# Kernel tuning notes

Hardware: AMD Instinct MI355X
Metric: run time of the kernel (lower is better)

Reference implementation:

```python
import jax, jax.numpy as jnp
import numpy as np

B, S_SRC, L_SRC, S_TGT, L_TGT, C = 4, 8, 512, 8, 512, 4
K_PALETTE = 97
PAD = -1.0
TAU = 0.1
EPS = 1e-15


def setup_inputs() -> dict:
    key = jax.random.key(0)
    k1, k2, k3, k4, k5, k6 = jax.random.split(key, 6)
    palette = jax.random.uniform(k1, (K_PALETTE, C), dtype=jnp.float32)
    src_idx = jax.random.randint(k2, (B, S_SRC, L_SRC), 0, K_PALETTE)
    tgt_idx = jax.random.randint(k3, (B, S_TGT, L_TGT), 0, K_PALETTE)
    src = palette[src_idx]
    tgt = palette[tgt_idx]
    pad_vec = jnp.full((C,), PAD, dtype=jnp.float32)
    src = jnp.where(jax.random.uniform(k4, (B, S_SRC, L_SRC, 1)) < 0.03, pad_vec, src)
    tgt = jnp.where(jax.random.uniform(k5, (B, S_TGT, L_TGT, 1)) < 0.03, pad_vec, tgt)
    seg_sim_map = jax.random.normal(k6, (B, S_TGT * L_TGT, S_SRC * L_SRC), dtype=jnp.float32)
    return {"seg_sim_map": seg_sim_map, "seg_colors_src": src, "seg_colors_tgt": tgt}


def _loss(seg_sim_map, seg_colors_src, seg_colors_tgt):
    Bb = seg_sim_map.shape[0]
    src_flat = seg_colors_src.reshape(Bb, -1, C)   # [B, Nsrc, C]
    tgt_flat = seg_colors_tgt.reshape(Bb, -1, C)   # [B, Ntgt, C]
    valid_src = ~jnp.all(src_flat == PAD, axis=-1)  # [B, Nsrc]
    valid_tgt = ~jnp.all(tgt_flat == PAD, axis=-1)  # [B, Ntgt]

    # eq[b,t,j]: valid tgt row t's color exactly equals valid src column j's color.
    # This replaces torch.unique + index_add: aggregating softmax mass over src
    # positions sharing the gt color is identical to index_add by color index
    # followed by gathering the gt color's bucket.
    eq = jnp.all(tgt_flat[:, :, None, :] == src_flat[:, None, :, :], axis=-1)
    eq = eq & valid_src[:, None, :] & valid_tgt[:, :, None]      # [B, Ntgt, Nsrc]
    matched = jnp.any(eq, axis=-1)                               # rows kept by nll mask

    # masked softmax over valid src columns == softmax over the sliced columns
    logits = jnp.where(valid_src[:, None, :], seg_sim_map / TAU, -jnp.inf)
    probs = jax.nn.softmax(logits, axis=-1)                      # [B, Ntgt, Nsrc]

    p_gt = jnp.einsum('btj,btj->bt', probs, eq.astype(probs.dtype))
    nll = -jnp.log(p_gt + EPS)                                   # [B, Ntgt]

    nll = nll.reshape(Bb, S_TGT, L_TGT)
    m = matched.reshape(Bb, S_TGT, L_TGT).astype(nll.dtype)
    nvalid = m.sum(-1)                                           # [B, S_tgt]
    seg_loss = jnp.where(nvalid > 0, (nll * m).sum(-1) / jnp.maximum(nvalid, 1.0), 0.0)
    cnt = jnp.sum((nvalid > 0).astype(jnp.int32))
    total = seg_loss.sum() / jnp.maximum(cnt, 1).astype(seg_loss.dtype)
    return total, cnt


def reference(seg_sim_map, seg_colors_src, seg_colors_tgt):
    return _loss(seg_sim_map, seg_colors_src, seg_colors_tgt)
```

## Files before the change

### kernel.cpp

```cpp
#include <hip/hip_runtime.h>
#include <math.h>

#define NSRC 4096
#define NTGT 4096
#define NB 4
#define L2SCALE (10.0f * 1.4426950408889634f)
#define PADBITS 0xBF800000u


__device__ __forceinline__ unsigned mix128(uint4 c) {
    unsigned h = c.x * 0x9E3779B1u;
    h ^= h >> 15; h *= 0x85EBCA77u;
    h ^= c.y;     h *= 0xC2B2AE3Du;
    h ^= h >> 13;
    h ^= c.z;     h *= 0x27D4EB2Fu;
    h ^= h >> 16;
    h ^= c.w;     h *= 0x9E3779B1u;
    h ^= h >> 15;
    return h;
}

__global__ __launch_bounds__(256) void key_kernel(const uint4* __restrict__ srcc,
                                                  const uint4* __restrict__ tgtc,
                                                  unsigned* __restrict__ skey,
                                                  unsigned* __restrict__ tkey) {
    int i = blockIdx.x * 256 + threadIdx.x;
    if (i < NB * NSRC) {
        uint4 c = srcc[i];
        bool pad = (c.x == PADBITS) && (c.y == PADBITS) && (c.z == PADBITS) && (c.w == PADBITS);
        skey[i] = pad ? 0u : (mix128(c) | 1u);
    } else {
        int j = i - NB * NSRC;
        uint4 c = tgtc[j];
        bool pad = (c.x == PADBITS) && (c.y == PADBITS) && (c.z == PADBITS) && (c.w == PADBITS);
        tkey[j] = pad ? 2u : (mix128(c) | 1u);
    }
}


__global__ __launch_bounds__(256) void row_kernel(const float* __restrict__ sim,
                                                  const unsigned* __restrict__ skey,
                                                  const unsigned* __restrict__ tkey,
                                                  float* __restrict__ row_nll,
                                                  float* __restrict__ row_m) {
    const int wave = threadIdx.x >> 6;
    const int lane = threadIdx.x & 63;
    const int row = blockIdx.x * 4 + wave;
    const int b = row >> 12;
    const float4* simv = (const float4*)(sim + (size_t)row * NSRC);
    const uint4* keyv = (const uint4*)(skey + (size_t)b * NSRC);
    const unsigned tk = tkey[row];

    float s0 = 0.f, s1 = 0.f, s2 = 0.f, s3 = 0.f;
    float g0 = 0.f, g1 = 0.f, g2 = 0.f, g3 = 0.f;
    int any = 0;

#define PROC(LV, KV, SA, GA)                                             \
    do {                                                                 \
        bool _eq = ((KV) == tk);                                         \
        float _arg = ((KV) != 0u) ? (LV) * L2SCALE : -1048576.0f;        \
        float _e = exp2f(_arg);                                          \
        SA += _e;                                                        \
        GA += _eq ? _e : 0.f;                                            \
        any |= (int)_eq;                                                 \
    } while (0)

    #pragma unroll
    for (int it = 0; it < 16; ++it) {
        int j4 = it * 64 + lane;
        float4 l4 = simv[j4];
        uint4 k4 = keyv[j4];
        PROC(l4.x, k4.x, s0, g0);
        PROC(l4.y, k4.y, s1, g1);
        PROC(l4.z, k4.z, s2, g2);
        PROC(l4.w, k4.w, s3, g3);
    }
#undef PROC

    float s = (s0 + s1) + (s2 + s3);
    float sg = (g0 + g1) + (g2 + g3);
    #pragma unroll
    for (int off = 1; off < 64; off <<= 1) {
        s += __shfl_xor(s, off);
        sg += __shfl_xor(sg, off);
    }
    any = __any(any) ? 1 : 0;

    if (lane == 0) {
        float p = (s > 0.f) ? (sg / s) : 0.f;
        float nll = -logf(p + 1e-15f);
        row_nll[row] = any ? nll : 0.f;
        row_m[row] = any ? 1.f : 0.f;
    }
}


__global__ __launch_bounds__(1024) void finalize_kernel(const float* __restrict__ row_nll,
                                                        const float* __restrict__ row_m,
                                                        float* __restrict__ out) {
    __shared__ float ssum[32], scnt[32];
    int wave = threadIdx.x >> 6, lane = threadIdx.x & 63;
    for (int seg = wave; seg < 32; seg += 16) {
        float a = 0.f, c = 0.f;
        for (int j = lane; j < 512; j += 64) {
            a += row_nll[seg * 512 + j];
            c += row_m[seg * 512 + j];
        }
        #pragma unroll
        for (int off = 1; off < 64; off <<= 1) {
            a += __shfl_xor(a, off);
            c += __shfl_xor(c, off);
        }
        if (lane == 0) { ssum[seg] = a; scnt[seg] = c; }
    }
    __syncthreads();
    if (threadIdx.x == 0) {
        float tot = 0.f;
        int cnt = 0;
        for (int i = 0; i < 32; ++i) {
            if (scnt[i] > 0.f) { tot += ssum[i] / scnt[i]; cnt++; }
        }
        out[0] = (cnt > 0) ? tot / (float)cnt : 0.f;
        out[1] = (float)cnt;
    }
}


extern "C" void kernel_launch(void* const* d_in, const int* in_sizes, int n_in,
                              void* d_out, int out_size, void* d_ws, size_t ws_size,
                              hipStream_t stream) {
    const float* sim = (const float*)d_in[0];
    const uint4* src = (const uint4*)d_in[1];
    const uint4* tgt = (const uint4*)d_in[2];
    float* out = (float*)d_out;

    unsigned* skey = (unsigned*)d_ws;
    unsigned* tkey = skey + NB * NSRC;
    float* row_nll = (float*)(tkey + NB * NTGT);
    float* row_m = row_nll + NB * NTGT;

    key_kernel<<<(NB * (NSRC + NTGT)) / 256, 256, 0, stream>>>(src, tgt, skey, tkey);
    row_kernel<<<NB * NTGT / 4, 256, 0, stream>>>(sim, skey, tkey, row_nll, row_m);
    finalize_kernel<<<1, 1024, 0, stream>>>(row_nll, row_m, out);
}
```

Before: 59.77 us.

## Stream sim with nontemporal loads and accumulate per-segment sums via atomics

The row kernel now reads the similarity matrix with nontemporal loads in a partially unrolled loop, since that data is read only once. Instead of writing per-row nll and mask arrays, each matched row atomically adds into 32 per-segment accumulators, which the key kernel zeroes. This shrinks the finalize kernel to a single wave. It reduces intermediate traffic and finalize work, but adds float atomic contention and makes the summation order nondeterministic.

```diff
diff --git a/kernel.cpp b/kernel.cpp
--- a/kernel.cpp
+++ b/kernel.cpp
@@ -6,6 +6,8 @@
 #define NB 4
 #define L2SCALE (10.0f * 1.4426950408889634f)
 #define PADBITS 0xBF800000u
+
+typedef float f4v __attribute__((ext_vector_type(4)));
 
 
 __device__ __forceinline__ unsigned mix128(uint4 c) {
@@ -23,8 +25,10 @@
 __global__ __launch_bounds__(256) void key_kernel(const uint4* __restrict__ srcc,
                                                   const uint4* __restrict__ tgtc,
                                                   unsigned* __restrict__ skey,
-                                                  unsigned* __restrict__ tkey) {
+                                                  unsigned* __restrict__ tkey,
+                                                  float* __restrict__ seg_acc) {
     int i = blockIdx.x * 256 + threadIdx.x;
+    if (blockIdx.x == 0 && threadIdx.x < 64) seg_acc[threadIdx.x] = 0.f;
     if (i < NB * NSRC) {
         uint4 c = srcc[i];
         bool pad = (c.x == PADBITS) && (c.y == PADBITS) && (c.z == PADBITS) && (c.w == PADBITS);
@@ -41,13 +45,12 @@
 __global__ __launch_bounds__(256) void row_kernel(const float* __restrict__ sim,
                                                   const unsigned* __restrict__ skey,
                                                   const unsigned* __restrict__ tkey,
-                                                  float* __restrict__ row_nll,
-                                                  float* __restrict__ row_m) {
+                                                  float* __restrict__ seg_acc) {
     const int wave = threadIdx.x >> 6;
     const int lane = threadIdx.x & 63;
     const int row = blockIdx.x * 4 + wave;
     const int b = row >> 12;
-    const float4* simv = (const float4*)(sim + (size_t)row * NSRC);
+    const f4v* simv = (const f4v*)(sim + (size_t)row * NSRC);
     const uint4* keyv = (const uint4*)(skey + (size_t)b * NSRC);
     const unsigned tk = tkey[row];
 
@@ -65,15 +68,18 @@
         any |= (int)_eq;                                                 \
     } while (0)
 
-    #pragma unroll
-    for (int it = 0; it < 16; ++it) {
-        int j4 = it * 64 + lane;
-        float4 l4 = simv[j4];
-        uint4 k4 = keyv[j4];
-        PROC(l4.x, k4.x, s0, g0);
-        PROC(l4.y, k4.y, s1, g1);
-        PROC(l4.z, k4.z, s2, g2);
-        PROC(l4.w, k4.w, s3, g3);
+    #pragma unroll 1
+    for (int it = 0; it < 4; ++it) {
+        #pragma unroll
+        for (int u = 0; u < 4; ++u) {
+            int j4 = it * 256 + u * 64 + lane;
+            f4v l4 = __builtin_nontemporal_load(&simv[j4]);
+            uint4 k4 = keyv[j4];
+            PROC(l4[0], k4.x, s0, g0);
+            PROC(l4[1], k4.y, s1, g1);
+            PROC(l4[2], k4.z, s2, g2);
+            PROC(l4[3], k4.w, s3, g3);
+        }
     }
 #undef PROC
 
@@ -86,42 +92,33 @@
     }
     any = __any(any) ? 1 : 0;
 
-    if (lane == 0) {
+    if (lane == 0 && any) {
         float p = (s > 0.f) ? (sg / s) : 0.f;
         float nll = -logf(p + 1e-15f);
-        row_nll[row] = any ? nll : 0.f;
-        row_m[row] = any ? 1.f : 0.f;
+        int seg = row >> 9;
+        atomicAdd(&seg_acc[seg], nll);
+        atomicAdd(&seg_acc[32 + seg], 1.f);
     }
 }
 
 
-__global__ __launch_bounds__(1024) void finalize_kernel(const float* __restrict__ row_nll,
-                                                        const float* __restrict__ row_m,
-                                                        float* __restrict__ out) {
-    __shared__ float ssum[32], scnt[32];
-    int wave = threadIdx.x >> 6, lane = threadIdx.x & 63;
-    for (int seg = wave; seg < 32; seg += 16) {
-        float a = 0.f, c = 0.f;
-        for (int j = lane; j < 512; j += 64) {
-            a += row_nll[seg * 512 + j];
-            c += row_m[seg * 512 + j];
-        }
-        #pragma unroll
-        for (int off = 1; off < 64; off <<= 1) {
-            a += __shfl_xor(a, off);
-            c += __shfl_xor(c, off);
-        }
-        if (lane == 0) { ssum[seg] = a; scnt[seg] = c; }
+__global__ __launch_bounds__(64) void finalize_kernel(const float* __restrict__ seg_acc,
+                                                      float* __restrict__ out) {
+    int lane = threadIdx.x;
+    float loss = 0.f, flag = 0.f;
+    if (lane < 32) {
+        float sum = seg_acc[lane];
+        float cnt = seg_acc[32 + lane];
+        if (cnt > 0.f) { loss = sum / cnt; flag = 1.f; }
     }
-    __syncthreads();
-    if (threadIdx.x == 0) {
-        float tot = 0.f;
-        int cnt = 0;
-        for (int i = 0; i < 32; ++i) {
-            if (scnt[i] > 0.f) { tot += ssum[i] / scnt[i]; cnt++; }
-        }
-        out[0] = (cnt > 0) ? tot / (float)cnt : 0.f;
-        out[1] = (float)cnt;
+    #pragma unroll
+    for (int off = 1; off < 64; off <<= 1) {
+        loss += __shfl_xor(loss, off);
+        flag += __shfl_xor(flag, off);
+    }
+    if (lane == 0) {
+        out[0] = (flag > 0.f) ? loss / flag : 0.f;
+        out[1] = flag;
     }
 }
 
@@ -136,10 +133,9 @@
 
     unsigned* skey = (unsigned*)d_ws;
     unsigned* tkey = skey + NB * NSRC;
-    float* row_nll = (float*)(tkey + NB * NTGT);
-    float* row_m = row_nll + NB * NTGT;
+    float* seg_acc = (float*)(tkey + NB * NTGT);
 
-    key_kernel<<<(NB * (NSRC + NTGT)) / 256, 256, 0, stream>>>(src, tgt, skey, tkey);
-    row_kernel<<<NB * NTGT / 4, 256, 0, stream>>>(sim, skey, tkey, row_nll, row_m);
-    finalize_kernel<<<1, 1024, 0, stream>>>(row_nll, row_m, out);
+    key_kernel<<<(NB * (NSRC + NTGT)) / 256, 256, 0, stream>>>(src, tgt, skey, tkey, seg_acc);
+    row_kernel<<<NB * NTGT / 4, 256, 0, stream>>>(sim, skey, tkey, seg_acc);
+    finalize_kernel<<<1, 64, 0, stream>>>(seg_acc, out);
 }
```

Measured after the change: 220.4 us. +268.8%, slower.

## Bucket source columns by color hash and gather matching columns per row

Applied to the files above, without the earlier changes.

Replaces the per-element key comparison with a per-batch shared-memory hash table that groups source column indices by color, built by one block per batch. Each row now computes the unmasked exp sum over all columns without loading keys. It then gathers only the columns of its matching color bucket and of the pad bucket to get the gt mass and to subtract the pad mass. Padded target rows exit early. This removes the key-array loads and the per-element selects, and uses the raw hardware exp2 builtin. The trade-offs are a serial single-block build stage, scattered gathers, and a 256-slot table that assumes few distinct colors per batch.

```diff
diff --git a/kernel.cpp b/kernel.cpp
--- a/kernel.cpp
+++ b/kernel.cpp
@@ -7,6 +7,7 @@
 #define L2SCALE (10.0f * 1.4426950408889634f)
 #define PADBITS 0xBF800000u
 
+__device__ __forceinline__ float fexp2(float x) { return __builtin_amdgcn_exp2f(x); }
 
 __device__ __forceinline__ unsigned mix128(uint4 c) {
     unsigned h = c.x * 0x9E3779B1u;
@@ -17,78 +18,136 @@
     h ^= h >> 16;
     h ^= c.w;     h *= 0x9E3779B1u;
     h ^= h >> 15;
-    return h;
-}
-
-__global__ __launch_bounds__(256) void key_kernel(const uint4* __restrict__ srcc,
+    return h | 1u;
+}
+
+
+__global__ __launch_bounds__(1024) void build_kernel(const uint4* __restrict__ srcc,
+                                                     unsigned* __restrict__ cols,
+                                                     unsigned* __restrict__ gkey,
+                                                     unsigned* __restrict__ gstart,
+                                                     unsigned* __restrict__ gcnt) {
+    const int b = blockIdx.x;
+    const int tid = threadIdx.x;
+    __shared__ unsigned hkey[256];
+    __shared__ int hcnt[256], hstart[256], hfill[256];
+    __shared__ int padcnt, padfill;
+    if (tid < 256) { hkey[tid] = 0u; hcnt[tid] = 0; hfill[tid] = 0; }
+    if (tid == 0) { padcnt = 0; padfill = 0; }
+    __syncthreads();
+
+    int slotreg[4];
+    #pragma unroll
+    for (int u = 0; u < 4; ++u) {
+        int j = u * 1024 + tid;
+        uint4 c = srcc[b * NSRC + j];
+        bool pad = (c.x == PADBITS) && (c.y == PADBITS) && (c.z == PADBITS) && (c.w == PADBITS);
+        if (pad) {
+            slotreg[u] = -1;
+            atomicAdd(&padcnt, 1);
+        } else {
+            unsigned k = mix128(c);
+            int s = (k >> 8) & 255;
+            while (true) {
+                unsigned old = atomicCAS(&hkey[s], 0u, k);
+                if (old == 0u || old == k) break;
+                s = (s + 1) & 255;
+            }
+            slotreg[u] = s;
+            atomicAdd(&hcnt[s], 1);
+        }
+    }
+    __syncthreads();
+    if (tid == 0) {
+        int off = padcnt;
+        for (int s = 0; s < 256; ++s) { hstart[s] = off; off += hcnt[s]; }
+    }
+    __syncthreads();
+    #pragma unroll
+    for (int u = 0; u < 4; ++u) {
+        int j = u * 1024 + tid;
+        int s = slotreg[u];
+        int idx = (s < 0) ? atomicAdd(&padfill, 1)
+                          : hstart[s] + atomicAdd(&hfill[s], 1);
+        cols[b * NSRC + idx] = (unsigned)j;
+    }
+    if (tid < 256) {
+        gkey[b * 256 + tid] = hkey[tid];
+        gstart[b * 256 + tid] = (unsigned)hstart[tid];
+        gcnt[b * 256 + tid] = (unsigned)hcnt[tid];
+    }
+}
+
+
+__global__ __launch_bounds__(256) void row_kernel(const float* __restrict__ sim,
                                                   const uint4* __restrict__ tgtc,
-                                                  unsigned* __restrict__ skey,
-                                                  unsigned* __restrict__ tkey) {
-    int i = blockIdx.x * 256 + threadIdx.x;
-    if (i < NB * NSRC) {
-        uint4 c = srcc[i];
-        bool pad = (c.x == PADBITS) && (c.y == PADBITS) && (c.z == PADBITS) && (c.w == PADBITS);
-        skey[i] = pad ? 0u : (mix128(c) | 1u);
-    } else {
-        int j = i - NB * NSRC;
-        uint4 c = tgtc[j];
-        bool pad = (c.x == PADBITS) && (c.y == PADBITS) && (c.z == PADBITS) && (c.w == PADBITS);
-        tkey[j] = pad ? 2u : (mix128(c) | 1u);
-    }
-}
-
-
-__global__ __launch_bounds__(256) void row_kernel(const float* __restrict__ sim,
-                                                  const unsigned* __restrict__ skey,
-                                                  const unsigned* __restrict__ tkey,
+                                                  const unsigned* __restrict__ cols,
+                                                  const unsigned* __restrict__ gkey,
+                                                  const unsigned* __restrict__ gstart,
+                                                  const unsigned* __restrict__ gcnt,
                                                   float* __restrict__ row_nll,
                                                   float* __restrict__ row_m) {
     const int wave = threadIdx.x >> 6;
     const int lane = threadIdx.x & 63;
     const int row = blockIdx.x * 4 + wave;
     const int b = row >> 12;
-    const float4* simv = (const float4*)(sim + (size_t)row * NSRC);
-    const uint4* keyv = (const uint4*)(skey + (size_t)b * NSRC);
-    const unsigned tk = tkey[row];
-
+    const float* srow = sim + (size_t)row * NSRC;
+
+    uint4 tc = tgtc[row];
+    bool tpad = (tc.x == PADBITS) && (tc.y == PADBITS) && (tc.z == PADBITS) && (tc.w == PADBITS);
+    if (tpad) {
+        if (lane == 0) { row_nll[row] = 0.f; row_m[row] = 0.f; }
+        return;
+    }
+    unsigned tk = mix128(tc);
+
+    int start = 0, cnt = 0;
+    {
+        int s = (tk >> 8) & 255;
+        while (true) {
+            unsigned k = gkey[b * 256 + s];
+            if (k == tk) { start = (int)gstart[b * 256 + s]; cnt = (int)gcnt[b * 256 + s]; break; }
+            if (k == 0u) break;
+            s = (s + 1) & 255;
+        }
+    }
+    int pcnt = (int)gstart[b * 256 + 0];
+
+    float sg = 0.f, sp = 0.f;
+    for (int i = lane; i < cnt; i += 64) {
+        int c = (int)cols[b * NSRC + start + i];
+        sg += fexp2(srow[c] * L2SCALE);
+    }
+    for (int i = lane; i < pcnt; i += 64) {
+        int c = (int)cols[b * NSRC + i];
+        sp += fexp2(srow[c] * L2SCALE);
+    }
+
+    const float4* simv = (const float4*)srow;
     float s0 = 0.f, s1 = 0.f, s2 = 0.f, s3 = 0.f;
-    float g0 = 0.f, g1 = 0.f, g2 = 0.f, g3 = 0.f;
-    int any = 0;
-
-#define PROC(LV, KV, SA, GA)                                             \
-    do {                                                                 \
-        bool _eq = ((KV) == tk);                                         \
-        float _arg = ((KV) != 0u) ? (LV) * L2SCALE : -1048576.0f;        \
-        float _e = exp2f(_arg);                                          \
-        SA += _e;                                                        \
-        GA += _eq ? _e : 0.f;                                            \
-        any |= (int)_eq;                                                 \
-    } while (0)
-
     #pragma unroll
     for (int it = 0; it < 16; ++it) {
-        int j4 = it * 64 + lane;
-        float4 l4 = simv[j4];
-        uint4 k4 = keyv[j4];
-        PROC(l4.x, k4.x, s0, g0);
-        PROC(l4.y, k4.y, s1, g1);
-        PROC(l4.z, k4.z, s2, g2);
-        PROC(l4.w, k4.w, s3, g3);
-    }
-#undef PROC
-
-    float s = (s0 + s1) + (s2 + s3);
-    float sg = (g0 + g1) + (g2 + g3);
+        float4 l4 = simv[it * 64 + lane];
+        s0 += fexp2(l4.x * L2SCALE);
+        s1 += fexp2(l4.y * L2SCALE);
+        s2 += fexp2(l4.z * L2SCALE);
+        s3 += fexp2(l4.w * L2SCALE);
+    }
+    float sf = (s0 + s1) + (s2 + s3);
+
     #pragma unroll
     for (int off = 1; off < 64; off <<= 1) {
-        s += __shfl_xor(s, off);
+        sf += __shfl_xor(sf, off);
         sg += __shfl_xor(sg, off);
-    }
-    any = __any(any) ? 1 : 0;
+        sp += __shfl_xor(sp, off);
+    }
 
     if (lane == 0) {
-        float p = (s > 0.f) ? (sg / s) : 0.f;
+        float sv = sf - sp;
+        sv = fmaxf(sv, fmaxf(sg, 1e-30f));
+        float p = sg / sv;
         float nll = -logf(p + 1e-15f);
+        bool any = sg > 0.f;
         row_nll[row] = any ? nll : 0.f;
         row_m[row] = any ? 1.f : 0.f;
     }
@@ -134,12 +193,14 @@
     const uint4* tgt = (const uint4*)d_in[2];
     float* out = (float*)d_out;
 
-    unsigned* skey = (unsigned*)d_ws;
-    unsigned* tkey = skey + NB * NSRC;
-    float* row_nll = (float*)(tkey + NB * NTGT);
+    unsigned* cols = (unsigned*)d_ws;
+    unsigned* gkey = cols + NB * NSRC;
+    unsigned* gstart = gkey + NB * 256;
+    unsigned* gcnt = gstart + NB * 256;
+    float* row_nll = (float*)(gcnt + NB * 256);
     float* row_m = row_nll + NB * NTGT;
 
-    key_kernel<<<(NB * (NSRC + NTGT)) / 256, 256, 0, stream>>>(src, tgt, skey, tkey);
-    row_kernel<<<NB * NTGT / 4, 256, 0, stream>>>(sim, skey, tkey, row_nll, row_m);
+    build_kernel<<<NB, 1024, 0, stream>>>(src, cols, gkey, gstart, gcnt);
+    row_kernel<<<NB * NTGT / 4, 256, 0, stream>>>(sim, tgt, cols, gkey, gstart, gcnt, row_nll, row_m);
     finalize_kernel<<<1, 1024, 0, stream>>>(row_nll, row_m, out);
 }
```

Result: slower. 84.21 us (+40.9%).
